# Kernel optimization log

Hardware: AMD Instinct MI355X
Metric: run time of the kernel (lower is better)

## Reference

```python
import jax, jax.numpy as jnp
import numpy as np

TRANSLATION_SCALE = 1.0
ROTATION_SCALE = 0.1
EPS = 1e-05


def setup_inputs() -> dict:
    key = jax.random.key(0)
    uv = jax.random.normal(key, (2000000, 3), dtype=jnp.float32)
    return {"uv": uv}


def reference(uv):
    # uv: [B, 3] = [x, y, p_yaw]
    B = uv.shape[0]
    w = uv[:, 2] * ROTATION_SCALE                     # omega_z, [B]
    theta_sqr = w * w
    theta = jnp.sqrt(theta_sqr)                       # = |w|
    A = jnp.sin(theta) / (theta + EPS)                # sin(theta)/theta
    Bc = (1.0 - jnp.cos(theta)) / (theta_sqr + EPS)   # (1-cos)/theta^2
    C = (1.0 - A) / (theta_sqr + EPS)                 # (1-A)/theta^2

    # skew(w) for z-only rotation: [[0,-w,0],[w,0,0],[0,0,0]]
    zeros = jnp.zeros_like(w)
    skew = jnp.stack([
        jnp.stack([zeros, -w, zeros], axis=-1),
        jnp.stack([w, zeros, zeros], axis=-1),
        jnp.stack([zeros, zeros, zeros], axis=-1),
    ], axis=-2)                                        # [B,3,3]
    # skew @ skew = diag(-w^2, -w^2, 0)
    skew2 = jnp.stack([
        jnp.stack([-theta_sqr, zeros, zeros], axis=-1),
        jnp.stack([zeros, -theta_sqr, zeros], axis=-1),
        jnp.stack([zeros, zeros, zeros], axis=-1),
    ], axis=-2)                                        # [B,3,3]

    I3 = jnp.eye(3, dtype=uv.dtype)
    R = I3 + A[:, None, None] * skew + Bc[:, None, None] * skew2   # rotation [B,3,3]
    V = I3 + Bc[:, None, None] * skew + C[:, None, None] * skew2   # left-Jacobian-like [B,3,3]

    u = jnp.stack([uv[:, 0] * TRANSLATION_SCALE,
                   uv[:, 1] * TRANSLATION_SCALE,
                   zeros], axis=-1)                    # [B,3]
    t = jnp.einsum('bij,bj->bi', V, u)                 # translation [B,3]

    top = jnp.concatenate([R, t[:, :, None]], axis=-1) # [B,3,4]
    bottom = jnp.broadcast_to(jnp.array([0., 0., 0., 1.], dtype=uv.dtype), (B, 1, 4))
    return jnp.concatenate([top, bottom], axis=-2)     # [B,4,4]
```

## Files before the change

### kernel.cpp

```cpp
#include <hip/hip_runtime.h>


#define ROTATION_SCALE 0.1f
#define EPS_F 1e-5f

__global__ __launch_bounds__(256) void lie_se3_kernel(
    const float* __restrict__ uv, float4* __restrict__ out, int B) {
  __shared__ float4 smem[1024];

  int tid = threadIdx.x;
  int m = blockIdx.x * 256 + tid;

  float x = 0.0f, y = 0.0f, p = 0.0f;
  if (m < B) {
    x = uv[3 * m + 0];
    y = uv[3 * m + 1];
    p = uv[3 * m + 2];
  }

  float w = p * ROTATION_SCALE;
  float ts = w * w;
  float th = fabsf(w);
  float s = __sinf(th);
  float c = __cosf(th);
  float A  = s / (th + EPS_F);
  float Bc = (1.0f - c) / (ts + EPS_F);
  float C  = (1.0f - A) / (ts + EPS_F);

  float R00 = 1.0f - Bc * ts;
  float Aw  = A * w;
  float V00 = 1.0f - C * ts;
  float Bw  = Bc * w;
  float t0 = V00 * x - Bw * y;
  float t1 = Bw * x + V00 * y;

  smem[4 * tid + 0] = make_float4(R00, -Aw, 0.0f, t0);
  smem[4 * tid + 1] = make_float4(Aw, R00, 0.0f, t1);
  smem[4 * tid + 2] = make_float4(0.0f, 0.0f, 1.0f, 0.0f);
  smem[4 * tid + 3] = make_float4(0.0f, 0.0f, 0.0f, 1.0f);
  __syncthreads();

  long long base = (long long)blockIdx.x * 1024;
  long long limit = 4LL * B;
  #pragma unroll
  for (int k = 0; k < 4; ++k) {
    int idx = tid + k * 256;
    long long g = base + idx;
    if (g < limit) out[g] = smem[idx];
  }
}

extern "C" void kernel_launch(void* const* d_in, const int* in_sizes, int n_in,
                              void* d_out, int out_size, void* d_ws, size_t ws_size,
                              hipStream_t stream) {
  const float* uv = (const float*)d_in[0];
  float4* out = (float4*)d_out;
  int B = in_sizes[0] / 3;
  int block = 256;
  int grid = (B + block - 1) / block;
  lie_se3_kernel<<<grid, block, 0, stream>>>(uv, out, B);
}
```

Before: 140.9 us.

## Stage input via vectorized LDS loads, swizzle LDS output, use nontemporal stores

Loads the strided [B,3] input as coalesced float4 vectors into shared memory instead of three scalar strided loads per thread. Applies an XOR swizzle to the shared output buffer to reduce bank conflicts on the float4 writes. Output goes through nontemporal loads and stores with a fast path that skips bounds checks for full blocks. The aim is better DRAM efficiency on a memory-bound kernel, at the cost of an extra barrier and more complex indexing.

```diff
diff --git a/kernel.cpp b/kernel.cpp
--- a/kernel.cpp
+++ b/kernel.cpp
@@ -4,18 +4,41 @@
 #define ROTATION_SCALE 0.1f
 #define EPS_F 1e-5f
 
+typedef float f4 __attribute__((ext_vector_type(4)));
+
+#define SWZ(j) ((j) ^ (((j) >> 5) & 7))
+
 __global__ __launch_bounds__(256) void lie_se3_kernel(
-    const float* __restrict__ uv, float4* __restrict__ out, int B) {
-  __shared__ float4 smem[1024];
+    const f4* __restrict__ uv4, const float* __restrict__ uvf,
+    f4* __restrict__ out, int B, int nf4) {
+  __shared__ f4 s_in4[192];
+  __shared__ f4 s_out[1024];
 
-  int tid = threadIdx.x;
-  int m = blockIdx.x * 256 + tid;
+  const int tid = threadIdx.x;
+  const int blk = blockIdx.x;
 
-  float x = 0.0f, y = 0.0f, p = 0.0f;
-  if (m < B) {
-    x = uv[3 * m + 0];
-    y = uv[3 * m + 1];
-    p = uv[3 * m + 2];
+  if (tid < 192) {
+    int gi = blk * 192 + tid;
+    f4 v = (f4)(0.f);
+    if (gi < nf4) v = __builtin_nontemporal_load(&uv4[gi]);
+    s_in4[tid] = v;
+  }
+  __syncthreads();
+
+  const float* s_inf = reinterpret_cast<const float*>(s_in4);
+  const int m = blk * 256 + tid;
+  const int gf = 3 * m;
+  float x, y, p;
+  if (gf + 3 <= 4 * nf4) {
+    x = s_inf[3 * tid + 0];
+    y = s_inf[3 * tid + 1];
+    p = s_inf[3 * tid + 2];
+  } else if (m < B) {
+    x = uvf[gf + 0];
+    y = uvf[gf + 1];
+    p = uvf[gf + 2];
+  } else {
+    x = y = p = 0.f;
   }
 
   float w = p * ROTATION_SCALE;
@@ -23,40 +46,56 @@
   float th = fabsf(w);
   float s = __sinf(th);
   float c = __cosf(th);
-  float A  = s / (th + EPS_F);
+  float A = s / (th + EPS_F);
   float Bc = (1.0f - c) / (ts + EPS_F);
-  float C  = (1.0f - A) / (ts + EPS_F);
+  float C = (1.0f - A) / (ts + EPS_F);
 
   float R00 = 1.0f - Bc * ts;
-  float Aw  = A * w;
+  float Aw = A * w;
   float V00 = 1.0f - C * ts;
-  float Bw  = Bc * w;
+  float Bw = Bc * w;
   float t0 = V00 * x - Bw * y;
   float t1 = Bw * x + V00 * y;
 
-  smem[4 * tid + 0] = make_float4(R00, -Aw, 0.0f, t0);
-  smem[4 * tid + 1] = make_float4(Aw, R00, 0.0f, t1);
-  smem[4 * tid + 2] = make_float4(0.0f, 0.0f, 1.0f, 0.0f);
-  smem[4 * tid + 3] = make_float4(0.0f, 0.0f, 0.0f, 1.0f);
+  const int j0 = 4 * tid;
+  {
+    f4 r0 = {R00, -Aw, 0.f, t0};
+    f4 r1 = {Aw, R00, 0.f, t1};
+    f4 r2 = {0.f, 0.f, 1.f, 0.f};
+    f4 r3 = {0.f, 0.f, 0.f, 1.f};
+    s_out[SWZ(j0 + 0)] = r0;
+    s_out[SWZ(j0 + 1)] = r1;
+    s_out[SWZ(j0 + 2)] = r2;
+    s_out[SWZ(j0 + 3)] = r3;
+  }
   __syncthreads();
 
-  long long base = (long long)blockIdx.x * 1024;
-  long long limit = 4LL * B;
-  #pragma unroll
-  for (int k = 0; k < 4; ++k) {
-    int idx = tid + k * 256;
-    long long g = base + idx;
-    if (g < limit) out[g] = smem[idx];
+  const int base = blk * 1024;
+  const int limit = 4 * B;
+  if (base + 1024 <= limit) {
+#pragma unroll
+    for (int k = 0; k < 4; ++k) {
+      int idx = tid + k * 256;
+      __builtin_nontemporal_store(s_out[SWZ(idx)], &out[base + idx]);
+    }
+  } else {
+#pragma unroll
+    for (int k = 0; k < 4; ++k) {
+      int idx = tid + k * 256;
+      if (base + idx < limit)
+        __builtin_nontemporal_store(s_out[SWZ(idx)], &out[base + idx]);
+    }
   }
 }
 
 extern "C" void kernel_launch(void* const* d_in, const int* in_sizes, int n_in,
                               void* d_out, int out_size, void* d_ws, size_t ws_size,
                               hipStream_t stream) {
-  const float* uv = (const float*)d_in[0];
-  float4* out = (float4*)d_out;
+  const float* uvf = (const float*)d_in[0];
+  const f4* uv4 = (const f4*)d_in[0];
+  f4* out = (f4*)d_out;
   int B = in_sizes[0] / 3;
-  int block = 256;
-  int grid = (B + block - 1) / block;
-  lie_se3_kernel<<<grid, block, 0, stream>>>(uv, out, B);
+  int nf4 = in_sizes[0] / 4;
+  int grid = (B + 255) / 256;
+  lie_se3_kernel<<<grid, 256, 0, stream>>>(uv4, uvf, out, B, nf4);
 }
```

Result: slower. 145.0 us (+2.9%).

## Replace LDS transpose with wave shuffles in a grid-stride loop

Applied to the files above, without the earlier changes.

Removes the shared-memory staging and block barrier. Each wave now builds its coalesced float4 output rows directly with __shfl cross-lane exchanges, and a grid-stride loop over 64-row tiles with a capped grid lets waves process several tiles. Exact divisions are also swapped for __fdividef. This trades LDS traffic and syncs for more shuffle and select instructions; the capped grid may reduce memory-level parallelism on this write-bound kernel.

```diff
diff --git a/kernel.cpp b/kernel.cpp
--- a/kernel.cpp
+++ b/kernel.cpp
@@ -4,49 +4,60 @@
 #define ROTATION_SCALE 0.1f
 #define EPS_F 1e-5f
 
+typedef float f4 __attribute__((ext_vector_type(4)));
+
 __global__ __launch_bounds__(256) void lie_se3_kernel(
-    const float* __restrict__ uv, float4* __restrict__ out, int B) {
-  __shared__ float4 smem[1024];
+    const float* __restrict__ uv, f4* __restrict__ out, int B) {
+  const int lane = threadIdx.x & 63;
+  const int wid = (blockIdx.x * blockDim.x + threadIdx.x) >> 6;
+  const int nwav = (gridDim.x * blockDim.x) >> 6;
+  const int ntile = (B + 63) >> 6;
+  const int lim4 = 4 * B;
 
-  int tid = threadIdx.x;
-  int m = blockIdx.x * 256 + tid;
+  for (int t = wid; t < ntile; t += nwav) {
+    int m = (t << 6) + lane;
+    float x = 0.f, y = 0.f, p = 0.f;
+    if (m < B) {
+      int g = 3 * m;
+      x = uv[g + 0];
+      y = uv[g + 1];
+      p = uv[g + 2];
+    }
 
-  float x = 0.0f, y = 0.0f, p = 0.0f;
-  if (m < B) {
-    x = uv[3 * m + 0];
-    y = uv[3 * m + 1];
-    p = uv[3 * m + 2];
-  }
+    float w = p * ROTATION_SCALE;
+    float ts = w * w;
+    float th = fabsf(w);
+    float sn = __sinf(th);
+    float cs = __cosf(th);
+    float A = __fdividef(sn, th + EPS_F);
+    float Bc = __fdividef(1.0f - cs, ts + EPS_F);
+    float C = __fdividef(1.0f - A, ts + EPS_F);
 
-  float w = p * ROTATION_SCALE;
-  float ts = w * w;
-  float th = fabsf(w);
-  float s = __sinf(th);
-  float c = __cosf(th);
-  float A  = s / (th + EPS_F);
-  float Bc = (1.0f - c) / (ts + EPS_F);
-  float C  = (1.0f - A) / (ts + EPS_F);
+    float R00 = 1.0f - Bc * ts;
+    float Aw = A * w;
+    float V00 = 1.0f - C * ts;
+    float Bw = Bc * w;
+    float t0 = V00 * x - Bw * y;
+    float t1 = Bw * x + V00 * y;
 
-  float R00 = 1.0f - Bc * ts;
-  float Aw  = A * w;
-  float V00 = 1.0f - C * ts;
-  float Bw  = Bc * w;
-  float t0 = V00 * x - Bw * y;
-  float t1 = Bw * x + V00 * y;
-
-  smem[4 * tid + 0] = make_float4(R00, -Aw, 0.0f, t0);
-  smem[4 * tid + 1] = make_float4(Aw, R00, 0.0f, t1);
-  smem[4 * tid + 2] = make_float4(0.0f, 0.0f, 1.0f, 0.0f);
-  smem[4 * tid + 3] = make_float4(0.0f, 0.0f, 0.0f, 1.0f);
-  __syncthreads();
-
-  long long base = (long long)blockIdx.x * 1024;
-  long long limit = 4LL * B;
-  #pragma unroll
-  for (int k = 0; k < 4; ++k) {
-    int idx = tid + k * 256;
-    long long g = base + idx;
-    if (g < limit) out[g] = smem[idx];
+    const int gbase = t << 8;
+    const int r = lane & 3;
+    const bool full = (gbase + 256) <= lim4;
+#pragma unroll
+    for (int k = 0; k < 4; ++k) {
+      int src = 16 * k + (lane >> 2);
+      float a = __shfl(R00, src, 64);
+      float b = __shfl(Aw, src, 64);
+      float c0 = __shfl(t0, src, 64);
+      float d0 = __shfl(t1, src, 64);
+      f4 v;
+      v.x = (r == 0) ? a : ((r == 1) ? b : 0.f);
+      v.y = (r == 0) ? -b : ((r == 1) ? a : 0.f);
+      v.z = (r == 2) ? 1.f : 0.f;
+      v.w = (r == 0) ? c0 : ((r == 1) ? d0 : ((r == 3) ? 1.f : 0.f));
+      int gi = gbase + 64 * k + lane;
+      if (full || gi < lim4) out[gi] = v;
+    }
   }
 }
 
@@ -54,9 +65,10 @@
                               void* d_out, int out_size, void* d_ws, size_t ws_size,
                               hipStream_t stream) {
   const float* uv = (const float*)d_in[0];
-  float4* out = (float4*)d_out;
+  f4* out = (f4*)d_out;
   int B = in_sizes[0] / 3;
-  int block = 256;
-  int grid = (B + block - 1) / block;
-  lie_se3_kernel<<<grid, block, 0, stream>>>(uv, out, B);
+  int grid = (B + 255) / 256;
+  if (grid > 2048) grid = 2048;
+  if (grid < 1) grid = 1;
+  lie_se3_kernel<<<grid, 256, 0, stream>>>(uv, out, B);
 }
```

Result: slower. 146.6 us (+4.0%).
